# Kernel tuning notes

Measured on AMD Instinct MI355X. Metric: run time of the kernel, lower is better.

The kernel has to match this reference:

```python
import jax, jax.numpy as jnp
import numpy as np

T, B, DIM, N = 2, 256, 512, 196


def setup_inputs() -> dict:
    key = jax.random.key(0)
    ks = jax.random.split(key, 6)
    scale_mem = (2.0 / (DIM + DIM)) ** 0.5      # GlorotNormal
    scale_cat = (2.0 / (2 * DIM + DIM)) ** 0.5
    scale_attn = (2.0 / (DIM + 1)) ** 0.5
    return {
        "memory": jax.random.normal(ks[0], (T, B, DIM), dtype=jnp.float32),
        "know": jax.random.normal(ks[1], (B, DIM, N), dtype=jnp.float32),
        "control": jax.random.normal(ks[2], (T, B, DIM), dtype=jnp.float32),
        "W_mem": jax.random.normal(ks[3], (DIM, DIM), dtype=jnp.float32) * scale_mem,
        "b_mem": jnp.zeros((DIM,), dtype=jnp.float32),
        "W_concat": jax.random.normal(ks[4], (2 * DIM, DIM), dtype=jnp.float32) * scale_cat,
        "b_concat": jnp.zeros((DIM,), dtype=jnp.float32),
        "W_attn": jax.random.normal(ks[5], (DIM, 1), dtype=jnp.float32) * scale_attn,
        "b_attn": jnp.zeros((1,), dtype=jnp.float32),
    }


def reference(memory, know, control, W_mem, b_mem, W_concat, b_concat, W_attn, b_attn):
    # mem = Dense(dim)(memory[-1]) -> [B, dim]
    mem = memory[-1] @ W_mem + b_mem
    # mem[..., None] * know -> [B, dim, N]; concat along channel axis -> [B, 2*dim, N]
    cat = jnp.concatenate([mem[:, :, None] * know, know], axis=1)
    # transpose to [B, N, 2*dim], Dense(dim) -> [B, N, dim]
    concat = jnp.swapaxes(cat, 1, 2) @ W_concat + b_concat
    # gate by control[-1] -> [B, N, dim]; Dense(1) + squeeze -> [B, N]
    attn = concat * control[-1][:, None, :]
    logits = jnp.squeeze(attn @ W_attn, -1) + b_attn[0]
    # softmax over N, then (faithfully) weighted sum over the dim axis -> [B, N]
    a = jax.nn.softmax(logits, axis=1)[:, None, :]  # [B, 1, N]
    read = jnp.sum(a * know, axis=1)  # [B, N]
    return read
```

## Files before the change

kernel.cpp:

```cpp
#include <hip/hip_runtime.h>
#include <cfloat>

#define BB   256
#define DIM  512
#define NN   196
#define BT   16
#define IT   32

__global__ __launch_bounds__(1024, 1) void prep_kernel(
    const float* __restrict__ memory,
    const float* __restrict__ control,
    const float* __restrict__ W_mem,
    const float* __restrict__ b_mem,
    const float* __restrict__ W_concat,
    const float* __restrict__ W_attn,
    float* __restrict__ w_out)
{
    __shared__ float4 MU[8][DIM];
    __shared__ float  buf[12288];

    const int tid = threadIdx.x;
    const int il  = tid & 31;
    const int bg  = (tid >> 5) & 3;
    const int kg  = tid >> 7;
    const int b0  = blockIdx.x * BT;
    const int i0  = blockIdx.y * IT;

    const float* mem_in = memory  + (size_t)BB * DIM;
    const float* ctl_in = control + (size_t)BB * DIM;

    #pragma unroll
    for (int p4 = 0; p4 < 4; ++p4) {
        const int idx = p4 * 1024 + tid;
        const int k   = idx & 511;
        const int pp  = idx >> 9;
        const int bb  = b0 + pp * 2;
        const float wa = W_attn[k];
        MU[pp][k] = make_float4(
            mem_in[(size_t)bb       * DIM + k],
            ctl_in[(size_t)bb       * DIM + k] * wa,
            mem_in[(size_t)(bb + 1) * DIM + k],
            ctl_in[(size_t)(bb + 1) * DIM + k] * wa);
    }

    float am[4] = {0.f, 0.f, 0.f, 0.f};
    float a1[4] = {0.f, 0.f, 0.f, 0.f};
    float a2[4] = {0.f, 0.f, 0.f, 0.f};

    const int sr = tid >> 5;
    const int sc = tid & 15;
    const int h  = (tid >> 4) & 1;

    for (int kt = 0; kt < DIM; kt += 64) {
        __syncthreads();

        {
            const float4 q = *(const float4*)&W_concat[
                (size_t)(h * DIM + i0 + sr) * DIM + kt + sc * 4];
            const int kb = sc * 4;
            buf[((kb + 0) * 33 + sr) * 2 + h] = q.x;
            buf[((kb + 1) * 33 + sr) * 2 + h] = q.y;
            buf[((kb + 2) * 33 + sr) * 2 + h] = q.z;
            buf[((kb + 3) * 33 + sr) * 2 + h] = q.w;
        }
        __syncthreads();

        #pragma unroll
        for (int kk = 0; kk < 8; ++kk) {
            const int kl = kg * 8 + kk;
            const int k  = kt + kl;
            const float  wm  = W_mem[(size_t)k * DIM + i0 + il];
            const float2 c   = ((const float2*)buf)[kl * 33 + il];
            const float4 mu0 = MU[bg * 2 + 0][k];
            const float4 mu1 = MU[bg * 2 + 1][k];
            am[0] = fmaf(mu0.x, wm,  am[0]);
            a1[0] = fmaf(mu0.y, c.x, a1[0]);
            a2[0] = fmaf(mu0.y, c.y, a2[0]);
            am[1] = fmaf(mu0.z, wm,  am[1]);
            a1[1] = fmaf(mu0.w, c.x, a1[1]);
            a2[1] = fmaf(mu0.w, c.y, a2[1]);
            am[2] = fmaf(mu1.x, wm,  am[2]);
            a1[2] = fmaf(mu1.y, c.x, a1[2]);
            a2[2] = fmaf(mu1.y, c.y, a2[2]);
            am[3] = fmaf(mu1.z, wm,  am[3]);
            a1[3] = fmaf(mu1.w, c.x, a1[3]);
            a2[3] = fmaf(mu1.w, c.y, a2[3]);
        }
    }

    __syncthreads();
    #pragma unroll
    for (int j = 0; j < 4; ++j) {
        const int row = (kg * 16 + bg * 4 + j) * 32 + il;
        buf[row]        = am[j];
        buf[4096 + row] = a1[j];
        buf[8192 + row] = a2[j];
    }
    __syncthreads();
    if (tid < 512) {
        const int b = tid >> 5, ii = tid & 31;
        float sm = 0.f, s1 = 0.f, s2 = 0.f;
        #pragma unroll
        for (int t = 0; t < 8; ++t) {
            const int row = (t * 16 + b) * 32 + ii;
            sm += buf[row];
            s1 += buf[4096 + row];
            s2 += buf[8192 + row];
        }
        w_out[(size_t)(b0 + b) * DIM + i0 + ii] = (sm + b_mem[i0 + ii]) * s1 + s2;
    }
}

__global__ __launch_bounds__(1024) void read_kernel(
    const float* __restrict__ know,
    const float* __restrict__ w,
    float* __restrict__ out)
{
    __shared__ float  w_s[DIM];
    __shared__ float4 part_lg[16][50];
    __shared__ float4 part_ks[16][50];
    __shared__ float  tmp[256];
    __shared__ float  bc[2];

    const int tx  = threadIdx.x;
    const int ty  = threadIdx.y;
    const int tid = ty * 64 + tx;
    const int b   = blockIdx.x;

    if (tid < DIM) w_s[tid] = w[(size_t)b * DIM + tid];
    __syncthreads();

    float4 lg = make_float4(0.f, 0.f, 0.f, 0.f);
    float4 ks = make_float4(0.f, 0.f, 0.f, 0.f);
    if (tx < 49) {
        const float4* kp = (const float4*)(know + (size_t)b * DIM * NN) + (size_t)(ty * 32) * 49 + tx;
        const float*  wp = w_s + ty * 32;
        #pragma unroll 8
        for (int dd = 0; dd < 32; ++dd) {
            const float4 kv = kp[(size_t)dd * 49];
            const float  wv = wp[dd];
            lg.x = fmaf(kv.x, wv, lg.x); lg.y = fmaf(kv.y, wv, lg.y);
            lg.z = fmaf(kv.z, wv, lg.z); lg.w = fmaf(kv.w, wv, lg.w);
            ks.x += kv.x; ks.y += kv.y; ks.z += kv.z; ks.w += kv.w;
        }
        part_lg[ty][tx] = lg;
        part_ks[ty][tx] = ks;
    }
    __syncthreads();

    float lgn = 0.f, ksn = 0.f;
    if (tid < NN) {
        const int ng = tid >> 2, j = tid & 3;
        #pragma unroll
        for (int t = 0; t < 16; ++t) {
            lgn += ((const float*)&part_lg[t][ng])[j];
            ksn += ((const float*)&part_ks[t][ng])[j];
        }
    }

    if (tid < 256) tmp[tid] = (tid < NN) ? lgn : -FLT_MAX;
    __syncthreads();
    if (tid < 64) {
        float m = fmaxf(fmaxf(tmp[tid], tmp[tid + 64]),
                        fmaxf(tmp[tid + 128], tmp[tid + 192]));
        #pragma unroll
        for (int o = 32; o; o >>= 1) m = fmaxf(m, __shfl_down(m, o));
        if (tid == 0) bc[0] = m;
    }
    __syncthreads();

    const float e = (tid < NN) ? __expf(lgn - bc[0]) : 0.f;
    if (tid < 256) tmp[tid] = e;
    __syncthreads();
    if (tid < 64) {
        float s = tmp[tid] + tmp[tid + 64] + tmp[tid + 128] + tmp[tid + 192];
        #pragma unroll
        for (int o = 32; o; o >>= 1) s += __shfl_down(s, o);
        if (tid == 0) bc[1] = s;
    }
    __syncthreads();

    if (tid < NN) out[(size_t)b * NN + tid] = e / bc[1] * ksn;
}

extern "C" void kernel_launch(void* const* d_in, const int* in_sizes, int n_in,
                              void* d_out, int out_size, void* d_ws, size_t ws_size,
                              hipStream_t stream) {
    const float* memory   = (const float*)d_in[0];
    const float* know     = (const float*)d_in[1];
    const float* control  = (const float*)d_in[2];
    const float* W_mem    = (const float*)d_in[3];
    const float* b_mem    = (const float*)d_in[4];
    const float* W_concat = (const float*)d_in[5];
    const float* W_attn   = (const float*)d_in[7];
    float* w_ws = (float*)d_ws;
    float* outp = (float*)d_out;

    prep_kernel<<<dim3(BB / BT, DIM / IT), dim3(1024), 0, stream>>>(
        memory, control, W_mem, b_mem, W_concat, W_attn, w_ws);
    read_kernel<<<dim3(BB), dim3(64, 16), 0, stream>>>(know, w_ws, outp);
}
```

Before: 37.09 us.

## Split read kernel across two DIM slabs with separate softmax combine kernel

Splits the know-reduction kernel so each batch row is handled by two blocks, each covering half of the DIM axis, and writes partial logits and column sums to workspace. A new small combine kernel adds the partials and performs the softmax and final scaling. This doubles the block count (256 to 512) to raise occupancy on the memory-bound know read, at the cost of an extra kernel launch and a workspace round trip. It falls back to the old single kernel if the workspace is too small.

```diff
diff --git a/kernel.cpp b/kernel.cpp
--- a/kernel.cpp
+++ b/kernel.cpp
@@ -53,7 +53,6 @@
 
     for (int kt = 0; kt < DIM; kt += 64) {
         __syncthreads();
-
         {
             const float4 q = *(const float4*)&W_concat[
                 (size_t)(h * DIM + i0 + sr) * DIM + kt + sc * 4];
@@ -111,9 +110,101 @@
     }
 }
 
-__global__ __launch_bounds__(1024) void read_kernel(
+__global__ __launch_bounds__(1024, 2) void read_part(
     const float* __restrict__ know,
     const float* __restrict__ w,
+    float* __restrict__ part)
+{
+    __shared__ float  w_s[256];
+    __shared__ float4 plg[16][50];
+    __shared__ float4 pks[16][50];
+
+    const int tx   = threadIdx.x;
+    const int ty   = threadIdx.y;
+    const int tid  = ty * 64 + tx;
+    const int b    = blockIdx.x;
+    const int slab = blockIdx.y;
+
+    if (tid < 256) w_s[tid] = w[(size_t)b * DIM + slab * 256 + tid];
+    __syncthreads();
+
+    float4 lg = make_float4(0.f, 0.f, 0.f, 0.f);
+    float4 ks = make_float4(0.f, 0.f, 0.f, 0.f);
+    if (tx < 49) {
+        const float4* kp = (const float4*)(know + (size_t)b * DIM * NN)
+                         + (size_t)(slab * 256 + ty * 16) * 49 + tx;
+        const float*  wp = w_s + ty * 16;
+        #pragma unroll 8
+        for (int dd = 0; dd < 16; ++dd) {
+            const float4 kv = kp[(size_t)dd * 49];
+            const float  wv = wp[dd];
+            lg.x = fmaf(kv.x, wv, lg.x); lg.y = fmaf(kv.y, wv, lg.y);
+            lg.z = fmaf(kv.z, wv, lg.z); lg.w = fmaf(kv.w, wv, lg.w);
+            ks.x += kv.x; ks.y += kv.y; ks.z += kv.z; ks.w += kv.w;
+        }
+        plg[ty][tx] = lg;
+        pks[ty][tx] = ks;
+    }
+    __syncthreads();
+
+    if (tid < NN) {
+        const int ng = tid >> 2, j = tid & 3;
+        float lgn = 0.f, ksn = 0.f;
+        #pragma unroll
+        for (int t = 0; t < 16; ++t) {
+            lgn += ((const float*)&plg[t][ng])[j];
+            ksn += ((const float*)&pks[t][ng])[j];
+        }
+        float* pb = part + ((size_t)(b * 2 + slab) * 2) * NN;
+        pb[tid]      = lgn;
+        pb[NN + tid] = ksn;
+    }
+}
+
+__global__ __launch_bounds__(256) void combine_kernel(
+    const float* __restrict__ part,
+    float* __restrict__ out)
+{
+    __shared__ float tmp[256];
+    __shared__ float bc[2];
+
+    const int tid = threadIdx.x;
+    const int b   = blockIdx.x;
+    const float* pb = part + (size_t)b * 4 * NN;
+
+    float lg = 0.f, ks = 0.f;
+    if (tid < NN) {
+        lg = pb[tid] + pb[2 * NN + tid];
+        ks = pb[NN + tid] + pb[3 * NN + tid];
+    }
+
+    tmp[tid] = (tid < NN) ? lg : -FLT_MAX;
+    __syncthreads();
+    if (tid < 64) {
+        float m = fmaxf(fmaxf(tmp[tid], tmp[tid + 64]),
+                        fmaxf(tmp[tid + 128], tmp[tid + 192]));
+        #pragma unroll
+        for (int o = 32; o; o >>= 1) m = fmaxf(m, __shfl_down(m, o));
+        if (tid == 0) bc[0] = m;
+    }
+    __syncthreads();
+
+    const float e = (tid < NN) ? __expf(lg - bc[0]) : 0.f;
+    tmp[tid] = e;
+    __syncthreads();
+    if (tid < 64) {
+        float s = tmp[tid] + tmp[tid + 64] + tmp[tid + 128] + tmp[tid + 192];
+        #pragma unroll
+        for (int o = 32; o; o >>= 1) s += __shfl_down(s, o);
+        if (tid == 0) bc[1] = s;
+    }
+    __syncthreads();
+
+    if (tid < NN) out[(size_t)b * NN + tid] = e / bc[1] * ks;
+}
+
+__global__ __launch_bounds__(1024) void read_kernel(
+    const float* __restrict__ know, const float* __restrict__ w,
     float* __restrict__ out)
 {
     __shared__ float  w_s[DIM];
@@ -193,10 +284,21 @@
     const float* b_mem    = (const float*)d_in[4];
     const float* W_concat = (const float*)d_in[5];
     const float* W_attn   = (const float*)d_in[7];
+    float* outp = (float*)d_out;
+
+    const size_t W_BYTES    = (size_t)BB * DIM * sizeof(float);
+    const size_t PART_BYTES = (size_t)BB * 4 * NN * sizeof(float);
+
     float* w_ws = (float*)d_ws;
-    float* outp = (float*)d_out;
 
     prep_kernel<<<dim3(BB / BT, DIM / IT), dim3(1024), 0, stream>>>(
         memory, control, W_mem, b_mem, W_concat, W_attn, w_ws);
-    read_kernel<<<dim3(BB), dim3(64, 16), 0, stream>>>(know, w_ws, outp);
-}
+
+    if (ws_size >= W_BYTES + PART_BYTES) {
+        float* partp = (float*)((char*)d_ws + W_BYTES);
+        read_part<<<dim3(BB, 2), dim3(64, 16), 0, stream>>>(know, w_ws, partp);
+        combine_kernel<<<dim3(BB), dim3(256), 0, stream>>>(partp, outp);
+    } else {
+        read_kernel<<<dim3(BB), dim3(64, 16), 0, stream>>>(know, w_ws, outp);
+    }
+}
```

Measured after the change: 39.08 us. +5.4%, slower.
